# Kernel optimization log

Hardware: AMD Instinct MI355X
Metric: run time of the kernel (lower is better)

The kernel has to match this reference:

```python
import jax, jax.numpy as jnp
import numpy as np

MAX_EMBED = 1024
MAX_HEADS = 16
MIN_WIDTH_RATIO = 0.25


def setup_inputs() -> dict:
    key = jax.random.key(0)
    ks = jax.random.split(key, 10)
    B, S, E = 4, 1024, MAX_EMBED
    query = jax.random.normal(ks[0], (B, S, E), dtype=jnp.float32)
    attention_mask = jax.random.randint(ks[1], (B, 1, 1, S), 0, 2, dtype=jnp.int32)
    # SlimmableLinear params (max sizes); kaiming-ish scale ~ 1/sqrt(fan_in)
    scale = 1.0 / np.sqrt(E)
    def lin(kw, kb):
        w = jax.random.uniform(kw, (E, E), dtype=jnp.float32, minval=-scale, maxval=scale)
        b = jax.random.uniform(kb, (E,), dtype=jnp.float32, minval=-scale, maxval=scale)
        return w, b
    q_w, q_b = lin(ks[2], ks[3])
    k_w, k_b = lin(ks[4], ks[5])
    v_w, v_b = lin(ks[6], ks[7])
    o_w, o_b = lin(ks[8], ks[9])
    return {"query": query, "attention_mask": attention_mask,
            "q_w": q_w, "q_b": q_b, "k_w": k_w, "k_b": k_b,
            "v_w": v_w, "v_b": v_b, "o_w": o_w, "o_b": o_b,
            "width": 768}


def _slim_linear(x, w, b, width):
    # weight stored [out, in] like torch; slice to [width, width]
    return x[..., :width] @ w[:width, :width].T + b[:width]


def reference(query, attention_mask, q_w, q_b, k_w, k_b, v_w, v_b, o_w, o_b, width):
    min_width = int(MAX_EMBED * MIN_WIDTH_RATIO)
    width = max(min_width, min(int(width), MAX_EMBED))
    num_heads = max(1, width * MAX_HEADS // MAX_EMBED)
    head_dim = width // num_heads
    B, S, _ = query.shape

    q = _slim_linear(query, q_w, q_b, width)  # [B,S,width]
    k = _slim_linear(query, k_w, k_b, width)  # key=query (self-attn)
    v = _slim_linear(query, v_w, v_b, width)

    q = q.reshape(B, S, num_heads, head_dim).transpose(0, 2, 1, 3)  # [B,H,S,D]
    k = k.reshape(B, S, num_heads, head_dim).transpose(0, 2, 1, 3)
    v = v.reshape(B, S, num_heads, head_dim).transpose(0, 2, 1, 3)

    scores = jnp.einsum('bhqd,bhkd->bhqk', q, k) / jnp.sqrt(jnp.float32(head_dim))
    scores = jnp.where(attention_mask == 0, jnp.float32(-1e9), scores)
    attn_weights = jax.nn.softmax(scores, axis=-1)  # [B,H,S,S]
    attn_output = jnp.einsum('bhqk,bhkd->bhqd', attn_weights, v)
    attn_output = attn_output.transpose(0, 2, 1, 3).reshape(B, S, width)
    output = attn_output @ o_w[:width, :width].T + o_b[:width]
    return output, attn_weights
```

## Files before the change

kernel.cpp:

```cpp
#include <hip/hip_runtime.h>

#define Bn 4
#define Sn 1024
#define En 1024
#define Wn 768
#define Hn 12
#define Dn 64
#define XE ((size_t)Bn * Sn * Wn)

typedef __attribute__((ext_vector_type(8))) short short8;
typedef __attribute__((ext_vector_type(4))) short short4v;
typedef __attribute__((ext_vector_type(4))) float floatx4;

#define MFMA16(A, B, C) __builtin_amdgcn_mfma_f32_16x16x32_bf16(A, B, C, 0, 0, 0)

__device__ __forceinline__ unsigned short f2bf_rn(float f) {
    unsigned int u = __float_as_uint(f);
    unsigned int r = u + 0x7fffu + ((u >> 16) & 1u);
    return (unsigned short)(r >> 16);
}
__device__ __forceinline__ float bf2f(unsigned short h) {
    return __uint_as_float(((unsigned int)h) << 16);
}

__device__ __forceinline__ void gload_lds16(const unsigned short* g, unsigned short* l) {
    __builtin_amdgcn_global_load_lds(
        (const __attribute__((address_space(1))) void*)g,
        (__attribute__((address_space(3))) void*)l, 16, 0, 0);
}

__global__ __launch_bounds__(256) void prep_kernel(
    const float* __restrict__ x,
    const float* __restrict__ qw, const float* __restrict__ kw,
    const float* __restrict__ vw, const float* __restrict__ ow,
    const float* __restrict__ qb, const float* __restrict__ kb,
    const float* __restrict__ vb,
    unsigned short* __restrict__ xh, unsigned short* __restrict__ xl,
    unsigned short* __restrict__ wqh, unsigned short* __restrict__ wql,
    unsigned short* __restrict__ woh, unsigned short* __restrict__ wol,
    float* __restrict__ bq)
{
    const int bx = blockIdx.x;
    const float* src; unsigned short *dh, *dl; int e;
    bool lo = true;
    if (bx < 3072) {
        e = (bx * 256 + threadIdx.x) * 4;
        src = x; dh = xh; dl = xl; lo = false;
    } else if (bx < 3072 + 1728) {
        int bb = bx - 3072; int which = bb / 576;
        e = ((bb - which * 576) * 256 + threadIdx.x) * 4;
        src = (which == 0) ? qw : (which == 1) ? kw : vw;
        dh = wqh + (size_t)which * Wn * Wn;
        dl = wql + (size_t)which * Wn * Wn;
        lo = (which == 2);
    } else if (bx < 3072 + 1728 + 576) {
        e = ((bx - 3072 - 1728) * 256 + threadIdx.x) * 4;
        src = ow; dh = woh; dl = wol;
    } else {
        int t = (bx - 3072 - 1728 - 576) * 256 + threadIdx.x;
        if (t < Wn) bq[t] = qb[t];
        else if (t < 2 * Wn) bq[t] = kb[t - Wn];
        else if (t < 3 * Wn) bq[t] = vb[t - 2 * Wn];
        return;
    }
    int row = e / Wn, col = e - row * Wn;
    float4 v = *(const float4*)(src + (size_t)row * En + col);
    float f[4] = {v.x, v.y, v.z, v.w};
    short4v h, l;
    #pragma unroll
    for (int i = 0; i < 4; ++i) {
        unsigned short hh = f2bf_rn(f[i]);
        h[i] = (short)hh;
        l[i] = (short)f2bf_rn(f[i] - bf2f(hh));
    }
    *(short4v*)(dh + e) = h;
    if (lo) *(short4v*)(dl + e) = l;
}

__global__ __launch_bounds__(256) void qkv_mfma_kernel(
    const unsigned short* __restrict__ xh,
    const unsigned short* __restrict__ wh, const unsigned short* __restrict__ wl,
    const float* __restrict__ bq,
    unsigned short* __restrict__ qh_o, unsigned short* __restrict__ kh_o,
    unsigned short* __restrict__ vt_o)
{
    __shared__ __align__(16) unsigned short Ah[128 * 32];
    __shared__ __align__(16) unsigned short Bh[128 * 32];
    __shared__ __align__(16) unsigned short Bl[128 * 32];

    const int tid = threadIdx.x;
    const int wave = tid >> 6, lane = tid & 63;
    const int quad = lane >> 4, l16 = lane & 15;
    const int yy = ((int)blockIdx.y + 12) % 18;
    const int m0 = blockIdx.x * 128, n0 = yy * 128;
    const int wm = wave >> 1, wn = wave & 1;
    const int which = n0 / Wn;
    const bool full = (which == 2);

    floatx4 acc[4][4] = {};

    const int r_in = lane >> 2;
    const int cs = (lane & 3) ^ (r_in & 3);

    for (int k0 = 0; k0 < Wn; k0 += 32) {
        if (wave == 0) {
            #pragma unroll
            for (int i = 0; i < 8; ++i)
                gload_lds16(xh + (size_t)(m0 + i * 16 + r_in) * Wn + k0 + cs * 8,
                            Ah + i * 512);
        } else if (wave == 1) {
            #pragma unroll
            for (int i = 0; i < 8; ++i)
                gload_lds16(wh + (size_t)(n0 + i * 16 + r_in) * Wn + k0 + cs * 8,
                            Bh + i * 512);
        } else if (wave == 2 && full) {
            #pragma unroll
            for (int i = 0; i < 8; ++i)
                gload_lds16(wl + (size_t)(n0 + i * 16 + r_in) * Wn + k0 + cs * 8,
                            Bl + i * 512);
        }
        __syncthreads();

        short8 afh[4], bfh[4], bfl[4];
        #pragma unroll
        for (int t = 0; t < 4; ++t) {
            int mr = wm * 64 + t * 16 + l16;
            int ca = quad ^ (mr & 3);
            afh[t] = *(const short8*)(Ah + mr * 32 + ca * 8);
            int nr = wn * 64 + t * 16 + l16;
            int cb = quad ^ (nr & 3);
            bfh[t] = *(const short8*)(Bh + nr * 32 + cb * 8);
            if (full) bfl[t] = *(const short8*)(Bl + nr * 32 + cb * 8);
        }
        #pragma unroll
        for (int mt = 0; mt < 4; ++mt)
            #pragma unroll
            for (int nt = 0; nt < 4; ++nt) {
                acc[mt][nt] = MFMA16(afh[mt], bfh[nt], acc[mt][nt]);
                if (full) acc[mt][nt] = MFMA16(afh[mt], bfl[nt], acc[mt][nt]);
            }
        __syncthreads();
    }

    const int b = m0 >> 10;
    #pragma unroll
    for (int nt = 0; nt < 4; ++nt) {
        const int ng = n0 + wn * 64 + nt * 16 + l16;
        const float bias = bq[ng];
        const int f = ng - which * Wn;
        const int h = f >> 6, d = f & 63;
        #pragma unroll
        for (int mt = 0; mt < 4; ++mt) {
            const int mbase = m0 + wm * 64 + mt * 16 + quad * 4;
            const int s0 = mbase & (Sn - 1);
            if (which < 2) {
                unsigned short* oq = which ? kh_o : qh_o;
                size_t idx = (((size_t)(b * Hn + h)) * Sn + s0) * Dn + d;
                #pragma unroll
                for (int r = 0; r < 4; ++r)
                    oq[idx + (size_t)r * Dn] = f2bf_rn(acc[mt][nt][r] + bias);
            } else {
                size_t idx = (((size_t)(b * Hn + h)) * Dn + d) * Sn + s0;
                short4v pk;
                #pragma unroll
                for (int r = 0; r < 4; ++r)
                    pk[r] = (short)f2bf_rn(acc[mt][nt][r] + bias);
                *(short4v*)(vt_o + idx) = pk;
            }
        }
    }
}

__global__ __launch_bounds__(256) void attn_fused_kernel(
    const unsigned short* __restrict__ qh, const unsigned short* __restrict__ kh,
    const unsigned short* __restrict__ vt, const int* __restrict__ mask,
    float* __restrict__ attn, unsigned short* __restrict__ aoh)
{
    __shared__ __align__(16) char PsObuf[4 * 16 * 68 * 4];
    __shared__ float msk[Sn];
    __shared__ float Lsum[4][16];

    unsigned short (*Ps)[16 * 72] =
        (unsigned short (*)[16 * 72])PsObuf;
    float (*PsF)[16][68] = (float (*)[16][68])PsObuf;
    float (*Obuf)[16][68] = (float (*)[16][68])PsObuf;

    const int tid = threadIdx.x;
    const int wave = tid >> 6, lane = tid & 63;
    const int quad = lane >> 4, l16 = lane & 15;

    const int flat = (int)blockIdx.x + 64 * ((int)blockIdx.y + Hn * (int)blockIdx.z);
    const int logical = (flat & 7) * 384 + (flat >> 3);
    const int qt = logical & 63;
    const int bhg = logical >> 6;
    const int h = bhg % Hn, b = bhg / Hn;

    const int bh = b * Hn + h;
    const size_t kvb = (size_t)bh * Sn * Dn;
    const size_t vbase = (size_t)bh * Dn * Sn;

    {
        int4 mi = *(const int4*)(mask + b * Sn + tid * 4);
        msk[tid * 4 + 0] = (float)mi.x;
        msk[tid * 4 + 1] = (float)mi.y;
        msk[tid * 4 + 2] = (float)mi.z;
        msk[tid * 4 + 3] = (float)mi.w;
    }

    const int qrow = qt * 16 + l16;
    short8 qf[2];
    {
        const unsigned short* qp = qh + kvb + (size_t)qrow * Dn + quad * 8;
        qf[0] = *(const short8*)(qp);
        qf[1] = *(const short8*)(qp + 32);
    }
    __syncthreads();

    short8 Pr[8];
    float lsumr[4] = {0.f, 0.f, 0.f, 0.f};
    const int kbase = wave * 256;

    #pragma unroll
    for (int kk = 0; kk < 4; ++kk) {
        const int k0 = kbase + kk * 64;
        #pragma unroll
        for (int ct = 0; ct < 4; ++ct) {
            const int key = k0 + ct * 16 + l16;
            const unsigned short* kp = kh + kvb + (size_t)key * Dn + quad * 8;
            short8 kf0 = *(const short8*)(kp);
            short8 kf1 = *(const short8*)(kp + 32);
            floatx4 acc = {0.f, 0.f, 0.f, 0.f};
            acc = MFMA16(qf[0], kf0, acc);
            acc = MFMA16(qf[1], kf1, acc);
            const float mv = msk[key];
            #pragma unroll
            for (int r = 0; r < 4; ++r) {
                const float e = __expf(acc[r] * 0.125f) * mv;
                lsumr[r] += e;
                Ps[wave][(quad * 4 + r) * 72 + ct * 16 + l16] = f2bf_rn(e);
            }
        }
        Pr[kk * 2 + 0] = *(const short8*)&Ps[wave][l16 * 72 + quad * 8];
        Pr[kk * 2 + 1] = *(const short8*)&Ps[wave][l16 * 72 + 32 + quad * 8];
    }

    #pragma unroll
    for (int r = 0; r < 4; ++r) {
        float v = lsumr[r];
        v += __shfl_xor(v, 1, 64);
        v += __shfl_xor(v, 2, 64);
        v += __shfl_xor(v, 4, 64);
        v += __shfl_xor(v, 8, 64);
        lsumr[r] = v;
    }
    if (l16 == 0) {
        #pragma unroll
        for (int r = 0; r < 4; ++r) Lsum[wave][quad * 4 + r] = lsumr[r];
    }
    __syncthreads();

    float li[4];
    #pragma unroll
    for (int r = 0; r < 4; ++r) {
        const float lv = Lsum[0][quad * 4 + r] + Lsum[1][quad * 4 + r]
                       + Lsum[2][quad * 4 + r] + Lsum[3][quad * 4 + r];
        li[r] = (lv > 0.f) ? 1.f / lv : 0.f;
    }
    float lt;
    {
        const float lv = Lsum[0][l16] + Lsum[1][l16] + Lsum[2][l16] + Lsum[3][l16];
        lt = (lv > 0.f) ? 1.f / lv : 0.f;
    }

    floatx4 oacc[4] = {};
    float* abase = attn + ((size_t)bh * Sn + qt * 16) * Sn;

    #pragma unroll
    for (int kk = 0; kk < 4; ++kk) {
        const int k0 = kbase + kk * 64;
        #pragma unroll
        for (int ksp = 0; ksp < 2; ++ksp) {
            const short8 pf = Pr[kk * 2 + ksp];
            float4 f0, f1;
            f0.x = bf2f((unsigned short)pf[0]) * lt;
            f0.y = bf2f((unsigned short)pf[1]) * lt;
            f0.z = bf2f((unsigned short)pf[2]) * lt;
            f0.w = bf2f((unsigned short)pf[3]) * lt;
            f1.x = bf2f((unsigned short)pf[4]) * lt;
            f1.y = bf2f((unsigned short)pf[5]) * lt;
            f1.z = bf2f((unsigned short)pf[6]) * lt;
            f1.w = bf2f((unsigned short)pf[7]) * lt;
            *(float4*)&PsF[wave][l16][ksp * 32 + quad * 8]     = f0;
            *(float4*)&PsF[wave][l16][ksp * 32 + quad * 8 + 4] = f1;
            #pragma unroll
            for (int dt = 0; dt < 4; ++dt) {
                short8 vf = *(const short8*)(vt + vbase
                              + (size_t)(dt * 16 + l16) * Sn + k0 + ksp * 32 + quad * 8);
                oacc[dt] = MFMA16(pf, vf, oacc[dt]);
            }
        }
        #pragma unroll
        for (int rb = 0; rb < 4; ++rb) {
            float4 v4 = *(const float4*)&PsF[wave][rb * 4 + quad][l16 * 4];
            *(float4*)(abase + (size_t)(rb * 4 + quad) * Sn + k0 + l16 * 4) = v4;
        }
    }

    __syncthreads();
    if (wave != 0) {
        #pragma unroll
        for (int dt = 0; dt < 4; ++dt)
            #pragma unroll
            for (int r = 0; r < 4; ++r)
                Obuf[wave - 1][quad * 4 + r][dt * 16 + l16] = oacc[dt][r];
    }
    __syncthreads();
    if (wave == 0) {
        const int row0 = qt * 16 + quad * 4;
        #pragma unroll
        for (int dt = 0; dt < 4; ++dt)
            #pragma unroll
            for (int r = 0; r < 4; ++r) {
                const float o = (oacc[dt][r]
                               + Obuf[0][quad * 4 + r][dt * 16 + l16]
                               + Obuf[1][quad * 4 + r][dt * 16 + l16]
                               + Obuf[2][quad * 4 + r][dt * 16 + l16]) * li[r];
                const size_t idx = ((size_t)b * Sn + row0 + r) * Wn + h * Dn + dt * 16 + l16;
                aoh[idx] = f2bf_rn(o);
            }
    }
}

__global__ __launch_bounds__(256) void oproj_mfma_kernel(
    const unsigned short* __restrict__ aoh,
    const unsigned short* __restrict__ wh, const unsigned short* __restrict__ wl,
    const float* __restrict__ ob, float* __restrict__ out)
{
    __shared__ __align__(16) unsigned short Ah[64 * 32];
    __shared__ __align__(16) unsigned short Bh[128 * 32];
    __shared__ __align__(16) unsigned short Bl[128 * 32];

    const int tid = threadIdx.x;
    const int wave = tid >> 6, lane = tid & 63;
    const int quad = lane >> 4, l16 = lane & 15;

    const int flat = (int)blockIdx.x + 64 * (int)blockIdx.y;
    const int logical = (flat & 7) * 48 + (flat >> 3);
    const int m0 = (logical & 63) * 64, n0 = (logical >> 6) * 128;

    const int wm = wave >> 1, wn = wave & 1;

    floatx4 acc[2][4] = {};

    const int r_in = lane >> 2;
    const int cs = (lane & 3) ^ (r_in & 3);

    for (int k0 = 0; k0 < Wn; k0 += 32) {
        if (wave == 0) {
            #pragma unroll
            for (int i = 0; i < 4; ++i)
                gload_lds16(aoh + (size_t)(m0 + i * 16 + r_in) * Wn + k0 + cs * 8,
                            Ah + i * 512);
        } else if (wave == 1) {
            #pragma unroll
            for (int i = 0; i < 8; ++i)
                gload_lds16(wh + (size_t)(n0 + i * 16 + r_in) * Wn + k0 + cs * 8,
                            Bh + i * 512);
        } else if (wave == 2) {
            #pragma unroll
            for (int i = 0; i < 8; ++i)
                gload_lds16(wl + (size_t)(n0 + i * 16 + r_in) * Wn + k0 + cs * 8,
                            Bl + i * 512);
        }
        __syncthreads();

        short8 afh[2], bfh[4], bfl[4];
        #pragma unroll
        for (int t = 0; t < 2; ++t) {
            int mr = wm * 32 + t * 16 + l16;
            int ca = quad ^ (mr & 3);
            afh[t] = *(const short8*)(Ah + mr * 32 + ca * 8);
        }
        #pragma unroll
        for (int t = 0; t < 4; ++t) {
            int nr = wn * 64 + t * 16 + l16;
            int cb = quad ^ (nr & 3);
            bfh[t] = *(const short8*)(Bh + nr * 32 + cb * 8);
            bfl[t] = *(const short8*)(Bl + nr * 32 + cb * 8);
        }
        #pragma unroll
        for (int mt = 0; mt < 2; ++mt)
            #pragma unroll
            for (int nt = 0; nt < 4; ++nt) {
                acc[mt][nt] = MFMA16(afh[mt], bfh[nt], acc[mt][nt]);
                acc[mt][nt] = MFMA16(afh[mt], bfl[nt], acc[mt][nt]);
            }
        __syncthreads();
    }

    #pragma unroll
    for (int nt = 0; nt < 4; ++nt) {
        const int ng = n0 + wn * 64 + nt * 16 + l16;
        const float bias = ob[ng];
        #pragma unroll
        for (int mt = 0; mt < 2; ++mt) {
            const int m = m0 + wm * 32 + mt * 16 + quad * 4;
            #pragma unroll
            for (int r = 0; r < 4; ++r)
                out[(size_t)(m + r) * Wn + ng] = acc[mt][nt][r] + bias;
        }
    }
}

extern "C" void kernel_launch(void* const* d_in, const int* in_sizes, int n_in,
                              void* d_out, int out_size, void* d_ws, size_t ws_size,
                              hipStream_t stream) {
    const float* x    = (const float*)d_in[0];
    const int*   mask = (const int*)  d_in[1];
    const float* qw = (const float*)d_in[2];
    const float* qb = (const float*)d_in[3];
    const float* kw = (const float*)d_in[4];
    const float* kb = (const float*)d_in[5];
    const float* vw = (const float*)d_in[6];
    const float* vb = (const float*)d_in[7];
    const float* ow = (const float*)d_in[8];
    const float* ob = (const float*)d_in[9];

    float* out  = (float*)d_out;
    float* attn = out + XE;

    char* w = (char*)d_ws;
    unsigned short* xh   = (unsigned short*)w;  w += XE * 2;
    unsigned short* xl   = (unsigned short*)w;  w += XE * 2;
    unsigned short* wqh  = (unsigned short*)w;  w += (size_t)3 * Wn * Wn * 2;
    unsigned short* wql  = (unsigned short*)w;  w += (size_t)3 * Wn * Wn * 2;
    unsigned short* woh  = (unsigned short*)w;  w += (size_t)Wn * Wn * 2;
    unsigned short* wol  = (unsigned short*)w;  w += (size_t)Wn * Wn * 2;
    float*          bq   = (float*)w;           w += (size_t)3 * Wn * 4;
    unsigned short* qh   = (unsigned short*)w;  w += XE * 2;
    unsigned short* kh   = (unsigned short*)w;  w += XE * 2;
    unsigned short* vt_w = (unsigned short*)w;  w += XE * 2;

    prep_kernel<<<5385, 256, 0, stream>>>(x, qw, kw, vw, ow, qb, kb, vb,
                                          xh, xl, wqh, wql, woh, wol, bq);

    qkv_mfma_kernel<<<dim3(32, 18), 256, 0, stream>>>(
        xh, wqh, wql, bq, qh, kh, vt_w);

    attn_fused_kernel<<<dim3(64, Hn, Bn), 256, 0, stream>>>(
        qh, kh, vt_w, mask, attn, xh);

    oproj_mfma_kernel<<<dim3(64, 6), 256, 0, stream>>>(
        xh, woh, wol, ob, out);
}
```

Before: 371.8 us.

## Fuse Q and K projections per block sharing A tile, remap grid for XCD balance

Result: slower. 408.1 us (+9.8%).

```diff
diff --git a/kernel.cpp b/kernel.cpp
--- a/kernel.cpp
+++ b/kernel.cpp
@@ -91,13 +91,22 @@
     const int tid = threadIdx.x;
     const int wave = tid >> 6, lane = tid & 63;
     const int quad = lane >> 4, l16 = lane & 15;
-    const int yy = ((int)blockIdx.y + 12) % 18;
-    const int m0 = blockIdx.x * 128, n0 = yy * 128;
+
+    const int flat = (int)blockIdx.x + 32 * (int)blockIdx.y;
+    const int c = flat & 7, slot = flat >> 3;
+    const int m0 = ((c & 1) * 16 + (slot & 15)) * 128;
+    const int yy = (c >> 1) * 3 + (slot >> 4);
+    const bool isv = (yy >= 6);
+    const int n0 = (isv ? (yy - 6) : yy) * 128;
+
+    const unsigned short* gBh = wh + (size_t)(isv ? 2 : 0) * Wn * Wn + (size_t)n0 * Wn;
+    const unsigned short* gBl = isv ? (wl + (size_t)2 * Wn * Wn + (size_t)n0 * Wn)
+                                    : (wh + (size_t)1 * Wn * Wn + (size_t)n0 * Wn);
+
     const int wm = wave >> 1, wn = wave & 1;
-    const int which = n0 / Wn;
-    const bool full = (which == 2);
-
-    floatx4 acc[4][4] = {};
+
+    floatx4 acc0[4][4] = {};
+    floatx4 acc1[4][4] = {};
 
     const int r_in = lane >> 2;
     const int cs = (lane & 3) ^ (r_in & 3);
@@ -111,12 +120,12 @@
         } else if (wave == 1) {
             #pragma unroll
             for (int i = 0; i < 8; ++i)
-                gload_lds16(wh + (size_t)(n0 + i * 16 + r_in) * Wn + k0 + cs * 8,
+                gload_lds16(gBh + (size_t)(i * 16 + r_in) * Wn + k0 + cs * 8,
                             Bh + i * 512);
-        } else if (wave == 2 && full) {
+        } else if (wave == 2) {
             #pragma unroll
             for (int i = 0; i < 8; ++i)
-                gload_lds16(wl + (size_t)(n0 + i * 16 + r_in) * Wn + k0 + cs * 8,
+                gload_lds16(gBl + (size_t)(i * 16 + r_in) * Wn + k0 + cs * 8,
                             Bl + i * 512);
         }
         __syncthreads();
@@ -130,42 +139,54 @@
             int nr = wn * 64 + t * 16 + l16;
             int cb = quad ^ (nr & 3);
             bfh[t] = *(const short8*)(Bh + nr * 32 + cb * 8);
-            if (full) bfl[t] = *(const short8*)(Bl + nr * 32 + cb * 8);
-        }
-        #pragma unroll
-        for (int mt = 0; mt < 4; ++mt)
-            #pragma unroll
-            for (int nt = 0; nt < 4; ++nt) {
-                acc[mt][nt] = MFMA16(afh[mt], bfh[nt], acc[mt][nt]);
-                if (full) acc[mt][nt] = MFMA16(afh[mt], bfl[nt], acc[mt][nt]);
-            }
+            bfl[t] = *(const short8*)(Bl + nr * 32 + cb * 8);
+        }
+        if (isv) {
+            #pragma unroll
+            for (int mt = 0; mt < 4; ++mt)
+                #pragma unroll
+                for (int nt = 0; nt < 4; ++nt) {
+                    acc0[mt][nt] = MFMA16(afh[mt], bfh[nt], acc0[mt][nt]);
+                    acc0[mt][nt] = MFMA16(afh[mt], bfl[nt], acc0[mt][nt]);
+                }
+        } else {
+            #pragma unroll
+            for (int mt = 0; mt < 4; ++mt)
+                #pragma unroll
+                for (int nt = 0; nt < 4; ++nt) {
+                    acc0[mt][nt] = MFMA16(afh[mt], bfh[nt], acc0[mt][nt]);
+                    acc1[mt][nt] = MFMA16(afh[mt], bfl[nt], acc1[mt][nt]);
+                }
+        }
         __syncthreads();
     }
 
     const int b = m0 >> 10;
     #pragma unroll
     for (int nt = 0; nt < 4; ++nt) {
-        const int ng = n0 + wn * 64 + nt * 16 + l16;
-        const float bias = bq[ng];
-        const int f = ng - which * Wn;
+        const int f = n0 + wn * 64 + nt * 16 + l16;
         const int h = f >> 6, d = f & 63;
         #pragma unroll
         for (int mt = 0; mt < 4; ++mt) {
             const int mbase = m0 + wm * 64 + mt * 16 + quad * 4;
             const int s0 = mbase & (Sn - 1);
-            if (which < 2) {
-                unsigned short* oq = which ? kh_o : qh_o;
-                size_t idx = (((size_t)(b * Hn + h)) * Sn + s0) * Dn + d;
-                #pragma unroll
-                for (int r = 0; r < 4; ++r)
-                    oq[idx + (size_t)r * Dn] = f2bf_rn(acc[mt][nt][r] + bias);
-            } else {
+            if (isv) {
+                const float bias = bq[2 * Wn + f];
                 size_t idx = (((size_t)(b * Hn + h)) * Dn + d) * Sn + s0;
                 short4v pk;
                 #pragma unroll
                 for (int r = 0; r < 4; ++r)
-                    pk[r] = (short)f2bf_rn(acc[mt][nt][r] + bias);
+                    pk[r] = (short)f2bf_rn(acc0[mt][nt][r] + bias);
                 *(short4v*)(vt_o + idx) = pk;
+            } else {
+                const float biasq = bq[f];
+                const float biask = bq[Wn + f];
+                size_t idx = (((size_t)(b * Hn + h)) * Sn + s0) * Dn + d;
+                #pragma unroll
+                for (int r = 0; r < 4; ++r) {
+                    qh_o[idx + (size_t)r * Dn] = f2bf_rn(acc0[mt][nt][r] + biasq);
+                    kh_o[idx + (size_t)r * Dn] = f2bf_rn(acc1[mt][nt][r] + biask);
+                }
             }
         }
     }
@@ -444,7 +465,7 @@
     prep_kernel<<<5385, 256, 0, stream>>>(x, qw, kw, vw, ow, qb, kb, vb,
                                           xh, xl, wqh, wql, woh, wol, bq);
 
-    qkv_mfma_kernel<<<dim3(32, 18), 256, 0, stream>>>(
+    qkv_mfma_kernel<<<dim3(32, 12), 256, 0, stream>>>(
         xh, wqh, wql, bq, qh, kh, vt_w);
 
     attn_fused_kernel<<<dim3(64, Hn, Bn), 256, 0, stream>>>(
```
